# Performance work log

Hardware: AMD Instinct MI355X
Metric: run time of the kernel (lower is better)

The kernel has to match this reference:

```python
import jax, jax.numpy as jnp
import numpy as np

N_NODES = 100000
N_EDGES = 1600000
IN_DIM = 128
HID = 64


def _init_linear(key, fan_in, fan_out):
    kw, kb = jax.random.split(key)
    bound = 1.0 / np.sqrt(fan_in)
    W = jax.random.uniform(kw, (fan_in, fan_out), jnp.float32, -bound, bound)
    b = jax.random.uniform(kb, (fan_out,), jnp.float32, -bound, bound)
    return W, b


def setup_inputs() -> dict:
    key = jax.random.key(0)
    ks = jax.random.split(key, 6)
    x = jax.random.normal(ks[0], (N_NODES, IN_DIM), jnp.float32)
    edge_index = jax.random.randint(ks[1], (2, N_EDGES), 0, N_NODES, jnp.int64)
    W_pre, b_pre = _init_linear(ks[2], IN_DIM, HID)
    W1, b1 = _init_linear(ks[3], HID, HID)
    W2, b2 = _init_linear(ks[4], HID, HID)
    W3, b3 = _init_linear(ks[5], HID, HID)
    return {"x": x, "edge_index": edge_index, "W_pre": W_pre, "b_pre": b_pre,
            "W1": W1, "b1": b1, "W2": W2, "b2": b2, "W3": W3, "b3": b3}


def _gcn_layer(h, src, dst, dinv, W, b):
    # PyG GCNConv: h' = D^{-1/2} (A + I) D^{-1/2} (h W) + b, deg from A+I
    n = h.shape[0]
    hw = h @ W                                  # [N, out]
    norm = dinv[src] * dinv[dst]                # [E]
    msg = hw[src] * norm[:, None]               # gather + scale  [E, out]
    agg = jax.ops.segment_sum(msg, dst, num_segments=n)  # scatter-add
    agg = agg + hw * (dinv * dinv)[:, None]     # self-loop term (norm = dinv_i^2)
    return agg + b


def reference(x, edge_index, W_pre, b_pre, W1, b1, W2, b2, W3, b3):
    src, dst = edge_index[0], edge_index[1]
    n = x.shape[0]
    # degree of A + I (self loops added, as in GCNConv default)
    deg = jax.ops.segment_sum(jnp.ones(src.shape[0], x.dtype), dst, num_segments=n) + 1.0
    dinv = jax.lax.rsqrt(deg)

    h = x @ W_pre + b_pre                       # feature_pre linear
    h = jax.nn.relu(_gcn_layer(h, src, dst, dinv, W1, b1))  # dropout is identity in eval
    h = jax.nn.relu(_gcn_layer(h, src, dst, dinv, W2, b2))
    h = _gcn_layer(h, src, dst, dinv, W3, b3)
    # F.normalize(p=2, dim=-1) with eps=1e-12
    nrm = jnp.linalg.norm(h, axis=-1, keepdims=True)
    return h / jnp.maximum(nrm, 1e-12)
```

## Files before the change

kernel.cpp:

```cpp
#include <hip/hip_runtime.h>

#define N_NODES 100000
#define N_EDGES 1600000
#define IN_DIM 128
#define HID 64
#define NB 782
#define NBLK_GEMM 782
#define NGROUP 25000

typedef __attribute__((ext_vector_type(8))) _Float16 h8v;
typedef __attribute__((ext_vector_type(4))) float f4v;

struct Args {
  const float* x; const int* ei;
  const float* Wp; const float* bp;
  const float* W1; const float* b1;
  const float* W2; const float* b2;
  const float* W3; const float* b3;
  float* out;
  _Float16* bufA16; _Float16* hw16;
  int* pairs; int* csr; int* offs; float* dinv;
  int* bsz; int* bboff; int* bcur;
  _Float16* WpH; _Float16* WpL; _Float16* W1H; _Float16* W1L;
  _Float16* W2H; _Float16* W2L; _Float16* W3H; _Float16* W3L;
};

__device__ __forceinline__ void fmix_lo(float& acc, unsigned hv, float w) {
  asm("v_fma_mix_f32 %0, %1, %2, %0 op_sel:[0,0,0] op_sel_hi:[1,0,0]"
      : "+v"(acc) : "v"(hv), "v"(w));
}
__device__ __forceinline__ void fmix_hi(float& acc, unsigned hv, float w) {
  asm("v_fma_mix_f32 %0, %1, %2, %0 op_sel:[1,0,0] op_sel_hi:[1,0,0]"
      : "+v"(acc) : "v"(hv), "v"(w));
}

__device__ __forceinline__ void d_split(const float* __restrict__ W,
                                        _Float16* __restrict__ hi,
                                        _Float16* __restrict__ lo, int K, int i) {
  int k = i >> 6, n = i & 63;
  float v = W[i];
  _Float16 h = (_Float16)v;
  float r = v - (float)h;
  hi[n * K + k] = h;
  lo[n * K + k] = (_Float16)r;
}

__global__ __launch_bounds__(256) void f_prep(Args a) {
  int blk = blockIdx.x, t = threadIdx.x;
  if (blk < 32) d_split(a.Wp, a.WpH, a.WpL, IN_DIM, blk * 256 + t);
  else if (blk < 48) d_split(a.W1, a.W1H, a.W1L, HID, (blk - 32) * 256 + t);
  else if (blk < 64) d_split(a.W2, a.W2H, a.W2L, HID, (blk - 48) * 256 + t);
  else d_split(a.W3, a.W3H, a.W3L, HID, (blk - 64) * 256 + t);
}

__global__ __launch_bounds__(256) void f_bhist(Args a) {
  __shared__ int cnt[NB];
  int t = threadIdx.x;
  for (int i = t; i < NB; i += 256) cnt[i] = 0;
  __syncthreads();
  int e0 = blockIdx.x * 8192, e1 = min(e0 + 8192, N_EDGES);
  for (int e = e0 + t; e < e1; e += 256)
    atomicAdd(&cnt[a.ei[N_EDGES + e] >> 7], 1);
  __syncthreads();
  for (int i = t; i < NB; i += 256)
    if (cnt[i]) atomicAdd(&a.bsz[i], cnt[i]);
}

__global__ __launch_bounds__(256) void f_bscan(Args a) {
  __shared__ int sm[256];
  int t = threadIdx.x;
  int c[4];
  int idx0 = t * 4;
#pragma unroll
  for (int j = 0; j < 4; ++j) c[j] = (idx0 + j < NB) ? a.bsz[idx0 + j] : 0;
  int tsum = c[0] + c[1] + c[2] + c[3];
  int val = tsum;
  sm[t] = val;
  __syncthreads();
  for (int off = 1; off < 256; off <<= 1) {
    int u = (t >= off) ? sm[t - off] : 0;
    __syncthreads();
    val += u;
    sm[t] = val;
    __syncthreads();
  }
  int excl = val - tsum;
#pragma unroll
  for (int j = 0; j < 4; ++j) {
    int idx = idx0 + j;
    if (idx < NB) { a.bboff[idx] = excl; a.bcur[idx] = excl; }
    excl += c[j];
  }
  if (t == 255) a.bboff[NB] = val;
}

__global__ __launch_bounds__(256) void f_partition(Args a) {
  __shared__ int cnt[NB];
  __shared__ int base[NB];
  int t = threadIdx.x;
  for (int i = t; i < NB; i += 256) cnt[i] = 0;
  __syncthreads();
  int e0 = blockIdx.x * 8192, e1 = min(e0 + 8192, N_EDGES);
  for (int e = e0 + t; e < e1; e += 256)
    atomicAdd(&cnt[a.ei[N_EDGES + e] >> 7], 1);
  __syncthreads();
  for (int i = t; i < NB; i += 256) {
    int c = cnt[i];
    base[i] = c ? atomicAdd(&a.bcur[i], c) : 0;
    cnt[i] = 0;
  }
  __syncthreads();
  for (int e = e0 + t; e < e1; e += 256) {
    int s = a.ei[e];
    int d = a.ei[N_EDGES + e];
    int b = d >> 7;
    int r = atomicAdd(&cnt[b], 1);
    a.pairs[base[b] + r] = ((d & 127) << 17) | s;
  }
}

__global__ __launch_bounds__(256) void f_csrdeg(Args a) {
  __shared__ int ldeg[128];
  __shared__ int sc[128];
  __shared__ int lcur[128];
  int t = threadIdx.x;
  int b = blockIdx.x;
  int node0 = b << 7;
  int nloc = min(128, N_NODES - node0);
  int beg = a.bboff[b], end = a.bboff[b + 1];
  if (t < 128) ldeg[t] = 0;
  __syncthreads();
  for (int i = beg + t; i < end; i += 256)
    atomicAdd(&ldeg[(a.pairs[i] >> 17) & 127], 1);
  __syncthreads();
  int dv = (t < 128) ? ldeg[t] : 0;
  if (t < 128) sc[t] = dv;
  __syncthreads();
  for (int off = 1; off < 128; off <<= 1) {
    int u = (t >= off && t < 128) ? sc[t - off] : 0;
    __syncthreads();
    if (t < 128) sc[t] += u;
    __syncthreads();
  }
  if (t < nloc) {
    int o = beg + sc[t] - dv;
    a.offs[node0 + t] = o;
    lcur[t] = o;
    a.dinv[node0 + t] = rsqrtf((float)dv + 1.0f);
  }
  if (b == NB - 1 && t == 0) a.offs[N_NODES] = N_EDGES;
  __syncthreads();
  for (int i = beg + t; i < end; i += 256) {
    int p = a.pairs[i];
    int pos = atomicAdd(&lcur[(p >> 17) & 127], 1);
    a.csr[pos] = (p & 131071) << 7;
  }
}

__global__ __launch_bounds__(256) void f_gemm_pre(Args a) {
  __shared__ _Float16 sW[2 * 64 * IN_DIM];
  int t = threadIdx.x;
  int wave = t >> 6, lane = t & 63, fi = lane & 15, quad = lane >> 4;
  int r0 = blockIdx.x * 128 + wave * 32;

  f4v xb0[8], xb1[8];
  {
    int row = r0 + fi; if (row >= N_NODES) row = N_NODES - 1;
    const float* xp = a.x + (size_t)row * IN_DIM + quad * 8;
#pragma unroll
    for (int j = 0; j < 4; ++j) {
      xb0[2 * j]     = *(const f4v*)(xp + j * 32);
      xb0[2 * j + 1] = *(const f4v*)(xp + j * 32 + 4);
    }
  }
#pragma unroll
  for (int i = 0; i < 8; ++i) {
    int c = i * 256 + t;
    int h = c >> 10;
    int c2 = c & 1023;
    int n = c2 >> 4;
    const _Float16* src = (h ? a.WpL : a.WpH) + c2 * 8;
    f4v v = *(const f4v*)src;
    int off = (h << 14) | ((c2 * 16) ^ ((n & 7) << 4));
    *(f4v*)((char*)sW + off) = v;
  }
  __syncthreads();

  float bv[4];
#pragma unroll
  for (int ct = 0; ct < 4; ++ct) bv[ct] = a.bp[ct * 16 + fi];

#pragma unroll
  for (int f = 0; f < 2; ++f) {
    f4v* xcur = (f & 1) ? xb1 : xb0;
    f4v* xnxt = (f & 1) ? xb0 : xb1;
    if (f < 1) {
      int row = r0 + 16 + fi; if (row >= N_NODES) row = N_NODES - 1;
      const float* xp = a.x + (size_t)row * IN_DIM + quad * 8;
#pragma unroll
      for (int j = 0; j < 4; ++j) {
        xnxt[2 * j]     = *(const f4v*)(xp + j * 32);
        xnxt[2 * j + 1] = *(const f4v*)(xp + j * 32 + 4);
      }
    }
    f4v acc[4];
#pragma unroll
    for (int ct = 0; ct < 4; ++ct) acc[ct] = (f4v){0.f, 0.f, 0.f, 0.f};
#pragma unroll
    for (int k0i = 0; k0i < 4; ++k0i) {
      h8v ah, al;
#pragma unroll
      for (int j = 0; j < 4; ++j) {
        float v0 = xcur[2 * k0i][j], v1 = xcur[2 * k0i + 1][j];
        _Float16 h0 = (_Float16)v0, h1 = (_Float16)v1;
        ah[j] = h0;     al[j] = (_Float16)(v0 - (float)h0);
        ah[4 + j] = h1; al[4 + j] = (_Float16)(v1 - (float)h1);
      }
#pragma unroll
      for (int ct = 0; ct < 4; ++ct) {
        int n = ct * 16 + fi;
        int bo = ((n * IN_DIM + k0i * 32 + quad * 8) * 2) ^ ((n & 7) << 4);
        h8v bh = *(const h8v*)((const char*)sW + bo);
        h8v bl = *(const h8v*)((const char*)sW + 16384 + bo);
        acc[ct] = __builtin_amdgcn_mfma_f32_16x16x32_f16(ah, bh, acc[ct], 0, 0, 0);
        acc[ct] = __builtin_amdgcn_mfma_f32_16x16x32_f16(al, bh, acc[ct], 0, 0, 0);
        acc[ct] = __builtin_amdgcn_mfma_f32_16x16x32_f16(ah, bl, acc[ct], 0, 0, 0);
      }
    }
    int ro = r0 + f * 16;
#pragma unroll
    for (int ct = 0; ct < 4; ++ct) {
#pragma unroll
      for (int j = 0; j < 4; ++j) {
        int orow = ro + quad * 4 + j;
        if (orow < N_NODES)
          a.bufA16[(size_t)orow * HID + ct * 16 + fi] = (_Float16)(acc[ct][j] + bv[ct]);
      }
    }
  }
}

__global__ __launch_bounds__(256) void f_gemm64(Args a, const _Float16* __restrict__ Wh,
                                                const _Float16* __restrict__ Wl) {
  int t = threadIdx.x;
  int wave = t >> 6, lane = t & 63, fi = lane & 15, quad = lane >> 4;
  int r0 = blockIdx.x * 128 + wave * 32;

  h8v a0[2], a1[2];
  {
    int row = r0 + fi; if (row >= N_NODES) row = N_NODES - 1;
    const _Float16* xp = a.bufA16 + (size_t)row * HID + quad * 8;
    a0[0] = *(const h8v*)xp;
    a0[1] = *(const h8v*)(xp + 32);
  }
  h8v Bh[2][4], Bl[2][4];
#pragma unroll
  for (int k0i = 0; k0i < 2; ++k0i)
#pragma unroll
    for (int ct = 0; ct < 4; ++ct) {
      size_t o = (size_t)(ct * 16 + fi) * HID + k0i * 32 + quad * 8;
      Bh[k0i][ct] = *(const h8v*)(Wh + o);
      Bl[k0i][ct] = *(const h8v*)(Wl + o);
    }

#pragma unroll
  for (int f = 0; f < 2; ++f) {
    h8v* av = (f & 1) ? a1 : a0;
    h8v* nx = (f & 1) ? a0 : a1;
    if (f < 1) {
      int row = r0 + 16 + fi; if (row >= N_NODES) row = N_NODES - 1;
      const _Float16* xp = a.bufA16 + (size_t)row * HID + quad * 8;
      nx[0] = *(const h8v*)xp;
      nx[1] = *(const h8v*)(xp + 32);
    }
    f4v acc[4];
#pragma unroll
    for (int ct = 0; ct < 4; ++ct) acc[ct] = (f4v){0.f, 0.f, 0.f, 0.f};
#pragma unroll
    for (int k0i = 0; k0i < 2; ++k0i)
#pragma unroll
      for (int ct = 0; ct < 4; ++ct) {
        acc[ct] = __builtin_amdgcn_mfma_f32_16x16x32_f16(av[k0i], Bh[k0i][ct], acc[ct], 0, 0, 0);
        acc[ct] = __builtin_amdgcn_mfma_f32_16x16x32_f16(av[k0i], Bl[k0i][ct], acc[ct], 0, 0, 0);
      }
    int ro = r0 + f * 16;
#pragma unroll
    for (int ct = 0; ct < 4; ++ct)
#pragma unroll
      for (int j = 0; j < 4; ++j) {
        int orow = ro + quad * 4 + j;
        if (orow < N_NODES)
          a.hw16[(size_t)orow * HID + ct * 16 + fi] = (_Float16)acc[ct][j];
      }
  }
}

template <int MODE>
__device__ __forceinline__ void d_agg(int grp, const _Float16* __restrict__ hw,
                                      const int* __restrict__ offs,
                                      const int* __restrict__ csr,
                                      const float* __restrict__ dinv,
                                      const float* __restrict__ bias,
                                      _Float16* __restrict__ out16,
                                      float* __restrict__ out32) {
  int node = grp * 4 + (threadIdx.x >> 6);
  int lane = threadIdx.x & 63;
  int oct = lane >> 3;
  int fi = lane & 7;
  float di = dinv[node];
  int beg = offs[node];
  int end = offs[node + 1];
  int lb = fi * 16;
  const char* hwb = (const char*)hw;

  float acc[8];
#pragma unroll
  for (int c = 0; c < 8; ++c) acc[c] = 0.f;

  if (oct == 0) {
    uint4 hv = *(const uint4*)(hwb + ((size_t)node << 7) + lb);
    fmix_lo(acc[0], hv.x, di); fmix_hi(acc[1], hv.x, di);
    fmix_lo(acc[2], hv.y, di); fmix_hi(acc[3], hv.y, di);
    fmix_lo(acc[4], hv.z, di); fmix_hi(acc[5], hv.z, di);
    fmix_lo(acc[6], hv.w, di); fmix_hi(acc[7], hv.w, di);
  }
  for (int e0 = beg + oct; e0 < end; e0 += 16) {
    int off0 = csr[e0];
    int e1 = e0 + 8;
    bool v1 = e1 < end;
    int off1 = csr[v1 ? e1 : beg];
    float w0 = dinv[(unsigned)off0 >> 7];
    float w1 = v1 ? dinv[(unsigned)off1 >> 7] : 0.0f;
    uint4 h0 = *(const uint4*)(hwb + (unsigned)off0 + lb);
    uint4 h1 = *(const uint4*)(hwb + (unsigned)off1 + lb);
    fmix_lo(acc[0], h0.x, w0); fmix_hi(acc[1], h0.x, w0);
    fmix_lo(acc[2], h0.y, w0); fmix_hi(acc[3], h0.y, w0);
    fmix_lo(acc[4], h0.z, w0); fmix_hi(acc[5], h0.z, w0);
    fmix_lo(acc[6], h0.w, w0); fmix_hi(acc[7], h0.w, w0);
    fmix_lo(acc[0], h1.x, w1); fmix_hi(acc[1], h1.x, w1);
    fmix_lo(acc[2], h1.y, w1); fmix_hi(acc[3], h1.y, w1);
    fmix_lo(acc[4], h1.z, w1); fmix_hi(acc[5], h1.z, w1);
    fmix_lo(acc[6], h1.w, w1); fmix_hi(acc[7], h1.w, w1);
  }
#pragma unroll
  for (int c = 0; c < 8; ++c) {
    float v = acc[c];
    v += __shfl_xor(v, 8);
    v += __shfl_xor(v, 16);
    v += __shfl_xor(v, 32);
    acc[c] = v;
  }
  if (oct == 0) {
#pragma unroll
    for (int c = 0; c < 8; ++c) acc[c] = acc[c] * di + bias[fi * 8 + c];
    if (MODE == 0) {
      h8v o;
#pragma unroll
      for (int c = 0; c < 8; ++c) o[c] = (_Float16)fmaxf(acc[c], 0.f);
      *(h8v*)(out16 + (size_t)node * HID + fi * 8) = o;
    } else {
      float ss = 0.f;
#pragma unroll
      for (int c = 0; c < 8; ++c) ss += acc[c] * acc[c];
      ss += __shfl_xor(ss, 1);
      ss += __shfl_xor(ss, 2);
      ss += __shfl_xor(ss, 4);
      float sc = 1.0f / fmaxf(sqrtf(ss), 1e-12f);
      f4v o0 = {acc[0] * sc, acc[1] * sc, acc[2] * sc, acc[3] * sc};
      f4v o1 = {acc[4] * sc, acc[5] * sc, acc[6] * sc, acc[7] * sc};
      *(f4v*)(out32 + (size_t)node * HID + fi * 8) = o0;
      *(f4v*)(out32 + (size_t)node * HID + fi * 8 + 4) = o1;
    }
  }
}

__global__ __launch_bounds__(256) void f_agg_relu(Args a, const float* bias) {
  d_agg<0>(blockIdx.x, a.hw16, a.offs, a.csr, a.dinv, bias, a.bufA16, nullptr);
}

__global__ __launch_bounds__(256) void f_agg_norm(Args a) {
  d_agg<1>(blockIdx.x, a.hw16, a.offs, a.csr, a.dinv, a.b3, nullptr, a.out);
}

extern "C" void kernel_launch(void* const* d_in, const int* in_sizes, int n_in,
                              void* d_out, int out_size, void* d_ws, size_t ws_size,
                              hipStream_t stream) {
  char* ws = (char*)d_ws;
  Args a;
  a.x  = (const float*)d_in[0];
  a.ei = (const int*)d_in[1];
  a.Wp = (const float*)d_in[2];  a.bp = (const float*)d_in[3];
  a.W1 = (const float*)d_in[4];  a.b1 = (const float*)d_in[5];
  a.W2 = (const float*)d_in[6];  a.b2 = (const float*)d_in[7];
  a.W3 = (const float*)d_in[8];  a.b3 = (const float*)d_in[9];
  a.out  = (float*)d_out;
  a.bufA16 = (_Float16*)(ws + 0);
  a.hw16   = (_Float16*)(ws + 12800000);
  a.pairs  = (int*)(ws + 25600000);
  a.csr    = (int*)(ws + 32000000);
  a.offs   = (int*)(ws + 38400000);
  a.dinv   = (float*)(ws + 38800016);
  a.bsz    = (int*)(ws + 39200016);
  a.bboff  = (int*)(ws + 39203152);
  a.bcur   = (int*)(ws + 39206288);
  a.WpH = (_Float16*)(ws + 39210000);
  a.WpL = (_Float16*)(ws + 39226384);
  a.W1H = (_Float16*)(ws + 39242768);
  a.W1L = (_Float16*)(ws + 39250960);
  a.W2H = (_Float16*)(ws + 39259152);
  a.W2L = (_Float16*)(ws + 39267344);
  a.W3H = (_Float16*)(ws + 39275536);
  a.W3L = (_Float16*)(ws + 39283728);

  (void)hipMemsetAsync(a.bsz, 0, NB * sizeof(int), stream);
  f_prep<<<80, 256, 0, stream>>>(a);
  f_bhist<<<196, 256, 0, stream>>>(a);
  f_bscan<<<1, 256, 0, stream>>>(a);
  f_partition<<<196, 256, 0, stream>>>(a);
  f_csrdeg<<<NB, 256, 0, stream>>>(a);
  f_gemm_pre<<<NBLK_GEMM, 256, 0, stream>>>(a);
  f_gemm64<<<NBLK_GEMM, 256, 0, stream>>>(a, a.W1H, a.W1L);
  f_agg_relu<<<NGROUP, 256, 0, stream>>>(a, a.b1);
  f_gemm64<<<NBLK_GEMM, 256, 0, stream>>>(a, a.W2H, a.W2L);
  f_agg_relu<<<NGROUP, 256, 0, stream>>>(a, a.b2);
  f_gemm64<<<NBLK_GEMM, 256, 0, stream>>>(a, a.W3H, a.W3L);
  f_agg_norm<<<NGROUP, 256, 0, stream>>>(a);
}
```

Baseline: 361.3 us.

## Reorder GCN layers to aggregate then transform, fusing aggregation with GEMM

Uses associativity (A·(hW) = (A·h)W) to aggregate the raw fp16 features first, then multiplies by W inside the same kernel via MFMA on a 16-node tile held in shared memory. Each 64x64 GEMM kernel launch and its intermediate hw16 write and read are removed, and the epilogue (bias, relu or L2 normalize) is applied after the fused GEMM. In exchange, aggregated values are split into fp16 hi/lo pairs for accuracy, each wave processes 4 nodes serially, and each block reloads W slices from global memory.

Measured after the change: 333.1 us. -7.8%, faster.

```diff
diff --git a/kernel.cpp b/kernel.cpp
--- a/kernel.cpp
+++ b/kernel.cpp
@@ -6,7 +6,7 @@
 #define HID 64
 #define NB 782
 #define NBLK_GEMM 782
-#define NGROUP 25000
+#define NGROUP16 6250
 
 typedef __attribute__((ext_vector_type(8))) _Float16 h8v;
 typedef __attribute__((ext_vector_type(4))) float f4v;
@@ -240,146 +240,124 @@
   }
 }
 
-__global__ __launch_bounds__(256) void f_gemm64(Args a, const _Float16* __restrict__ Wh,
-                                                const _Float16* __restrict__ Wl) {
-  int t = threadIdx.x;
-  int wave = t >> 6, lane = t & 63, fi = lane & 15, quad = lane >> 4;
-  int r0 = blockIdx.x * 128 + wave * 32;
-
-  h8v a0[2], a1[2];
-  {
-    int row = r0 + fi; if (row >= N_NODES) row = N_NODES - 1;
-    const _Float16* xp = a.bufA16 + (size_t)row * HID + quad * 8;
-    a0[0] = *(const h8v*)xp;
-    a0[1] = *(const h8v*)(xp + 32);
-  }
-  h8v Bh[2][4], Bl[2][4];
-#pragma unroll
-  for (int k0i = 0; k0i < 2; ++k0i)
-#pragma unroll
-    for (int ct = 0; ct < 4; ++ct) {
-      size_t o = (size_t)(ct * 16 + fi) * HID + k0i * 32 + quad * 8;
-      Bh[k0i][ct] = *(const h8v*)(Wh + o);
-      Bl[k0i][ct] = *(const h8v*)(Wl + o);
-    }
-
-#pragma unroll
-  for (int f = 0; f < 2; ++f) {
-    h8v* av = (f & 1) ? a1 : a0;
-    h8v* nx = (f & 1) ? a0 : a1;
-    if (f < 1) {
-      int row = r0 + 16 + fi; if (row >= N_NODES) row = N_NODES - 1;
-      const _Float16* xp = a.bufA16 + (size_t)row * HID + quad * 8;
-      nx[0] = *(const h8v*)xp;
-      nx[1] = *(const h8v*)(xp + 32);
-    }
-    f4v acc[4];
-#pragma unroll
-    for (int ct = 0; ct < 4; ++ct) acc[ct] = (f4v){0.f, 0.f, 0.f, 0.f};
-#pragma unroll
-    for (int k0i = 0; k0i < 2; ++k0i)
-#pragma unroll
-      for (int ct = 0; ct < 4; ++ct) {
-        acc[ct] = __builtin_amdgcn_mfma_f32_16x16x32_f16(av[k0i], Bh[k0i][ct], acc[ct], 0, 0, 0);
-        acc[ct] = __builtin_amdgcn_mfma_f32_16x16x32_f16(av[k0i], Bl[k0i][ct], acc[ct], 0, 0, 0);
+template <int MODE>
+__global__ __launch_bounds__(256) void f_aggw(Args a, const _Float16* __restrict__ hsrc,
+                                              const _Float16* __restrict__ Wh,
+                                              const _Float16* __restrict__ Wl,
+                                              const float* __restrict__ bias,
+                                              _Float16* __restrict__ out16,
+                                              float* __restrict__ out32) {
+  __shared__ char sG[2][2048];
+  __shared__ float sSS[4][16];
+  int t = threadIdx.x;
+  int wave = t >> 6, lane = t & 63, oct = lane >> 3, fi = lane & 7;
+  int node0 = blockIdx.x * 16;
+  const char* hwb = (const char*)hsrc;
+  int lb = fi * 16;
+
+  for (int n = 0; n < 4; ++n) {
+    int node = node0 + wave * 4 + n;
+    float di = a.dinv[node];
+    int beg = a.offs[node];
+    int end = a.offs[node + 1];
+    float acc[8];
+#pragma unroll
+    for (int c = 0; c < 8; ++c) acc[c] = 0.f;
+
+    if (oct == 0) {
+      uint4 hv = *(const uint4*)(hwb + ((size_t)node << 7) + lb);
+      fmix_lo(acc[0], hv.x, di); fmix_hi(acc[1], hv.x, di);
+      fmix_lo(acc[2], hv.y, di); fmix_hi(acc[3], hv.y, di);
+      fmix_lo(acc[4], hv.z, di); fmix_hi(acc[5], hv.z, di);
+      fmix_lo(acc[6], hv.w, di); fmix_hi(acc[7], hv.w, di);
+    }
+    for (int e0 = beg + oct; e0 < end; e0 += 16) {
+      int off0 = a.csr[e0];
+      int e1 = e0 + 8;
+      bool v1 = e1 < end;
+      int off1 = a.csr[v1 ? e1 : beg];
+      float w0 = a.dinv[(unsigned)off0 >> 7];
+      float w1 = v1 ? a.dinv[(unsigned)off1 >> 7] : 0.0f;
+      uint4 h0 = *(const uint4*)(hwb + (unsigned)off0 + lb);
+      uint4 h1 = *(const uint4*)(hwb + (unsigned)off1 + lb);
+      fmix_lo(acc[0], h0.x, w0); fmix_hi(acc[1], h0.x, w0);
+      fmix_lo(acc[2], h0.y, w0); fmix_hi(acc[3], h0.y, w0);
+      fmix_lo(acc[4], h0.z, w0); fmix_hi(acc[5], h0.z, w0);
+      fmix_lo(acc[6], h0.w, w0); fmix_hi(acc[7], h0.w, w0);
+      fmix_lo(acc[0], h1.x, w1); fmix_hi(acc[1], h1.x, w1);
+      fmix_lo(acc[2], h1.y, w1); fmix_hi(acc[3], h1.y, w1);
+      fmix_lo(acc[4], h1.z, w1); fmix_hi(acc[5], h1.z, w1);
+      fmix_lo(acc[6], h1.w, w1); fmix_hi(acc[7], h1.w, w1);
+    }
+#pragma unroll
+    for (int c = 0; c < 8; ++c) {
+      float v = acc[c];
+      v += __shfl_xor(v, 8);
+      v += __shfl_xor(v, 16);
+      v += __shfl_xor(v, 32);
+      acc[c] = v;
+    }
+    if (oct == 0) {
+      int row = wave * 4 + n;
+      h8v gh, gl;
+#pragma unroll
+      for (int c = 0; c < 8; ++c) {
+        float g = acc[c] * di;
+        _Float16 h = (_Float16)g;
+        gh[c] = h;
+        gl[c] = (_Float16)(g - (float)h);
       }
-    int ro = r0 + f * 16;
-#pragma unroll
-    for (int ct = 0; ct < 4; ++ct)
-#pragma unroll
-      for (int j = 0; j < 4; ++j) {
-        int orow = ro + quad * 4 + j;
-        if (orow < N_NODES)
-          a.hw16[(size_t)orow * HID + ct * 16 + fi] = (_Float16)acc[ct][j];
-      }
-  }
-}
-
-template <int MODE>
-__device__ __forceinline__ void d_agg(int grp, const _Float16* __restrict__ hw,
-                                      const int* __restrict__ offs,
-                                      const int* __restrict__ csr,
-                                      const float* __restrict__ dinv,
-                                      const float* __restrict__ bias,
-                                      _Float16* __restrict__ out16,
-                                      float* __restrict__ out32) {
-  int node = grp * 4 + (threadIdx.x >> 6);
-  int lane = threadIdx.x & 63;
-  int oct = lane >> 3;
-  int fi = lane & 7;
-  float di = dinv[node];
-  int beg = offs[node];
-  int end = offs[node + 1];
-  int lb = fi * 16;
-  const char* hwb = (const char*)hw;
-
-  float acc[8];
-#pragma unroll
-  for (int c = 0; c < 8; ++c) acc[c] = 0.f;
-
-  if (oct == 0) {
-    uint4 hv = *(const uint4*)(hwb + ((size_t)node << 7) + lb);
-    fmix_lo(acc[0], hv.x, di); fmix_hi(acc[1], hv.x, di);
-    fmix_lo(acc[2], hv.y, di); fmix_hi(acc[3], hv.y, di);
-    fmix_lo(acc[4], hv.z, di); fmix_hi(acc[5], hv.z, di);
-    fmix_lo(acc[6], hv.w, di); fmix_hi(acc[7], hv.w, di);
-  }
-  for (int e0 = beg + oct; e0 < end; e0 += 16) {
-    int off0 = csr[e0];
-    int e1 = e0 + 8;
-    bool v1 = e1 < end;
-    int off1 = csr[v1 ? e1 : beg];
-    float w0 = dinv[(unsigned)off0 >> 7];
-    float w1 = v1 ? dinv[(unsigned)off1 >> 7] : 0.0f;
-    uint4 h0 = *(const uint4*)(hwb + (unsigned)off0 + lb);
-    uint4 h1 = *(const uint4*)(hwb + (unsigned)off1 + lb);
-    fmix_lo(acc[0], h0.x, w0); fmix_hi(acc[1], h0.x, w0);
-    fmix_lo(acc[2], h0.y, w0); fmix_hi(acc[3], h0.y, w0);
-    fmix_lo(acc[4], h0.z, w0); fmix_hi(acc[5], h0.z, w0);
-    fmix_lo(acc[6], h0.w, w0); fmix_hi(acc[7], h0.w, w0);
-    fmix_lo(acc[0], h1.x, w1); fmix_hi(acc[1], h1.x, w1);
-    fmix_lo(acc[2], h1.y, w1); fmix_hi(acc[3], h1.y, w1);
-    fmix_lo(acc[4], h1.z, w1); fmix_hi(acc[5], h1.z, w1);
-    fmix_lo(acc[6], h1.w, w1); fmix_hi(acc[7], h1.w, w1);
-  }
-#pragma unroll
-  for (int c = 0; c < 8; ++c) {
-    float v = acc[c];
-    v += __shfl_xor(v, 8);
-    v += __shfl_xor(v, 16);
-    v += __shfl_xor(v, 32);
-    acc[c] = v;
-  }
-  if (oct == 0) {
-#pragma unroll
-    for (int c = 0; c < 8; ++c) acc[c] = acc[c] * di + bias[fi * 8 + c];
-    if (MODE == 0) {
-      h8v o;
-#pragma unroll
-      for (int c = 0; c < 8; ++c) o[c] = (_Float16)fmaxf(acc[c], 0.f);
-      *(h8v*)(out16 + (size_t)node * HID + fi * 8) = o;
-    } else {
-      float ss = 0.f;
-#pragma unroll
-      for (int c = 0; c < 8; ++c) ss += acc[c] * acc[c];
-      ss += __shfl_xor(ss, 1);
-      ss += __shfl_xor(ss, 2);
-      ss += __shfl_xor(ss, 4);
-      float sc = 1.0f / fmaxf(sqrtf(ss), 1e-12f);
-      f4v o0 = {acc[0] * sc, acc[1] * sc, acc[2] * sc, acc[3] * sc};
-      f4v o1 = {acc[4] * sc, acc[5] * sc, acc[6] * sc, acc[7] * sc};
-      *(f4v*)(out32 + (size_t)node * HID + fi * 8) = o0;
-      *(f4v*)(out32 + (size_t)node * HID + fi * 8 + 4) = o1;
-    }
-  }
-}
-
-__global__ __launch_bounds__(256) void f_agg_relu(Args a, const float* bias) {
-  d_agg<0>(blockIdx.x, a.hw16, a.offs, a.csr, a.dinv, bias, a.bufA16, nullptr);
-}
-
-__global__ __launch_bounds__(256) void f_agg_norm(Args a) {
-  d_agg<1>(blockIdx.x, a.hw16, a.offs, a.csr, a.dinv, a.b3, nullptr, a.out);
+      int off = (row * 128 + fi * 16) ^ ((row & 7) << 4);
+      *(h8v*)(&sG[0][0] + off) = gh;
+      *(h8v*)(&sG[1][0] + off) = gl;
+    }
+  }
+  __syncthreads();
+
+  int r15 = lane & 15, quad = lane >> 4;
+  f4v acc4 = {0.f, 0.f, 0.f, 0.f};
+#pragma unroll
+  for (int k0i = 0; k0i < 2; ++k0i) {
+    int ao = (r15 * 128 + k0i * 64 + quad * 16) ^ ((r15 & 7) << 4);
+    h8v ah = *(const h8v*)(&sG[0][0] + ao);
+    h8v al = *(const h8v*)(&sG[1][0] + ao);
+    size_t bo = (size_t)(wave * 16 + r15) * HID + k0i * 32 + quad * 8;
+    h8v bh = *(const h8v*)(Wh + bo);
+    h8v bl = *(const h8v*)(Wl + bo);
+    acc4 = __builtin_amdgcn_mfma_f32_16x16x32_f16(ah, bh, acc4, 0, 0, 0);
+    acc4 = __builtin_amdgcn_mfma_f32_16x16x32_f16(al, bh, acc4, 0, 0, 0);
+    acc4 = __builtin_amdgcn_mfma_f32_16x16x32_f16(ah, bl, acc4, 0, 0, 0);
+  }
+  float bv = bias[wave * 16 + r15];
+  if (MODE == 0) {
+#pragma unroll
+    for (int j = 0; j < 4; ++j) {
+      int nl = quad * 4 + j;
+      out16[(size_t)(node0 + nl) * HID + wave * 16 + r15] =
+          (_Float16)fmaxf(acc4[j] + bv, 0.f);
+    }
+  } else {
+    float val[4], ssj[4];
+#pragma unroll
+    for (int j = 0; j < 4; ++j) { val[j] = acc4[j] + bv; ssj[j] = val[j] * val[j]; }
+#pragma unroll
+    for (int m = 1; m < 16; m <<= 1) {
+#pragma unroll
+      for (int j = 0; j < 4; ++j) ssj[j] += __shfl_xor(ssj[j], m);
+    }
+    if (r15 == 0) {
+#pragma unroll
+      for (int j = 0; j < 4; ++j) sSS[wave][quad * 4 + j] = ssj[j];
+    }
+    __syncthreads();
+#pragma unroll
+    for (int j = 0; j < 4; ++j) {
+      int nl = quad * 4 + j;
+      float tot = sSS[0][nl] + sSS[1][nl] + sSS[2][nl] + sSS[3][nl];
+      float sc = 1.0f / fmaxf(sqrtf(tot), 1e-12f);
+      out32[(size_t)(node0 + nl) * HID + wave * 16 + r15] = val[j] * sc;
+    }
+  }
 }
 
 extern "C" void kernel_launch(void* const* d_in, const int* in_sizes, int n_in,
@@ -419,10 +397,7 @@
   f_partition<<<196, 256, 0, stream>>>(a);
   f_csrdeg<<<NB, 256, 0, stream>>>(a);
   f_gemm_pre<<<NBLK_GEMM, 256, 0, stream>>>(a);
-  f_gemm64<<<NBLK_GEMM, 256, 0, stream>>>(a, a.W1H, a.W1L);
-  f_agg_relu<<<NGROUP, 256, 0, stream>>>(a, a.b1);
-  f_gemm64<<<NBLK_GEMM, 256, 0, stream>>>(a, a.W2H, a.W2L);
-  f_agg_relu<<<NGROUP, 256, 0, stream>>>(a, a.b2);
-  f_gemm64<<<NBLK_GEMM, 256, 0, stream>>>(a, a.W3H, a.W3L);
-  f_agg_norm<<<NGROUP, 256, 0, stream>>>(a);
-}
+  f_aggw<0><<<NGROUP16, 256, 0, stream>>>(a, a.bufA16, a.W1H, a.W1L, a.b1, a.hw16, nullptr);
+  f_aggw<0><<<NGROUP16, 256, 0, stream>>>(a, a.hw16, a.W2H, a.W2L, a.b2, a.bufA16, nullptr);
+  f_aggw<1><<<NGROUP16, 256, 0, stream>>>(a, a.bufA16, a.W3H, a.W3L, a.b3, nullptr, a.out);
+}
```
